# Kernel optimization log

Measured on AMD Instinct MI355X. Metric: run time of the kernel, lower is better.

The kernel has to match this reference:

```python
import jax, jax.numpy as jnp
import numpy as np

N_NODES = 10000

def _gcn_norm(edges, n_nodes):
    # PyG GCNConv default: add self-loops, symmetric normalization D^-1/2 A_hat D^-1/2
    src, dst = edges[0], edges[1]
    loop = jnp.arange(n_nodes, dtype=src.dtype)
    src = jnp.concatenate([src, loop])
    dst = jnp.concatenate([dst, loop])
    deg = jax.ops.segment_sum(jnp.ones_like(dst, dtype=jnp.float32), dst, num_segments=n_nodes)
    dinv = jnp.where(deg > 0, jax.lax.rsqrt(deg), 0.0)
    norm = dinv[src] * dinv[dst]  # [E + N]
    return src, dst, norm

def _gcn_layer(x, src, dst, norm, W, b):
    # linear transform, then gather -> weight -> scatter-add aggregation
    x = x @ W  # [N, F]
    msg = x[src] * norm[:, None]  # [E+N, F]
    out = jax.ops.segment_sum(msg, dst, num_segments=x.shape[0])
    return out + b

def setup_inputs() -> dict:
    key = jax.random.key(0)
    k1, k2, k3, k4 = jax.random.split(key, 4)
    d = 128
    E = 640000
    scale = 1.0 / np.sqrt(d)
    return {
        "nodes_embeddings": jax.random.normal(k1, (N_NODES, d), dtype=jnp.float32),
        "edges": jax.random.randint(k2, (2, E), 0, N_NODES, dtype=jnp.int64),
        "W1": jax.random.normal(k3, (d, d), dtype=jnp.float32) * scale,
        "b1": jnp.zeros((d,), dtype=jnp.float32),
        "W2": jax.random.normal(k4, (d, d), dtype=jnp.float32) * scale,
        "b2": jnp.zeros((d,), dtype=jnp.float32),
    }

def reference(nodes_embeddings, edges, W1, b1, W2, b2):
    src, dst, norm = _gcn_norm(edges, nodes_embeddings.shape[0])
    x = _gcn_layer(nodes_embeddings, src, dst, norm, W1, b1)
    x = _gcn_layer(x, src, dst, norm, W2, b2)
    return x
```

## Files before the change

### kernel.cpp

```cpp
#include <hip/hip_runtime.h>
#include <hip/hip_bf16.h>

#define D 128
#define NBINS 157
#define BIN_CAP 5120
#define EPB 4096
#define SCAP 96
#define SLABW (NBINS * SCAP)

__device__ __forceinline__ unsigned rne_bf16(float f) {
    unsigned u = __float_as_uint(f);
    return (u + 0x7FFFu + ((u >> 16) & 1u)) >> 16;
}
__device__ __forceinline__ float bf16_lo(unsigned u) { return __uint_as_float(u << 16); }
__device__ __forceinline__ float bf16_hi(unsigned u) { return __uint_as_float(u & 0xFFFF0000u); }

__global__ __launch_bounds__(512) void fused_gemm_scatter(
        const float* __restrict__ X, const float* __restrict__ W,
        float* __restrict__ Y,
        const int* __restrict__ src, const int* __restrict__ dst,
        int* __restrict__ cntMat, int* __restrict__ binned,
        int E, int N, int gGemm) {
    __shared__ float smem[D * D];
    int tid = threadIdx.x;

    if ((int)blockIdx.x < gGemm) {
        {
            const float4* W4 = (const float4*)W;
            float4* Ws4 = (float4*)smem;
            #pragma unroll
            for (int i = 0; i < 8; ++i)
                Ws4[tid + 512 * i] = W4[tid + 512 * i];
        }
        __syncthreads();
        const float2* Ws2 = (const float2*)smem;
        int col2 = tid & 63;
        int wv   = __builtin_amdgcn_readfirstlane(tid >> 6);
        int row0 = blockIdx.x * 32 + wv * 4;
        if (row0 >= N) return;

        const float4* xr[4];
        #pragma unroll
        for (int r = 0; r < 4; ++r) {
            int rr = row0 + r; if (rr > N - 1) rr = N - 1;
            xr[r] = (const float4*)(X + (size_t)rr * D);
        }
        float accx[4] = {0.f, 0.f, 0.f, 0.f};
        float accy[4] = {0.f, 0.f, 0.f, 0.f};
        #pragma unroll 8
        for (int kb = 0; kb < 32; ++kb) {
            float4 xv[4];
            #pragma unroll
            for (int r = 0; r < 4; ++r) xv[r] = xr[r][kb];
            #pragma unroll
            for (int kk = 0; kk < 4; ++kk) {
                float2 w = Ws2[(4 * kb + kk) * 64 + col2];
                #pragma unroll
                for (int r = 0; r < 4; ++r) {
                    float xs = ((const float*)&xv[r])[kk];
                    accx[r] = fmaf(xs, w.x, accx[r]);
                    accy[r] = fmaf(xs, w.y, accy[r]);
                }
            }
        }
        #pragma unroll
        for (int r = 0; r < 4; ++r) {
            int rr = row0 + r;
            if (rr < N)
                ((float2*)Y)[(size_t)rr * 64 + col2] = make_float2(accx[r], accy[r]);
        }
    } else {
        int* cnt   = (int*)smem;
        int* loff  = cnt + 160;
        int* scur  = cnt + 320;
        int* stage = cnt + 480;
        for (int b = tid; b < NBINS; b += 512) cnt[b] = 0;
        __syncthreads();

        int bid = blockIdx.x - gGemm;
        int base = bid * EPB + tid * 8;
        int s[8], dl[8], bn[8];
        int ne = 0;
        if (base + 8 <= E) {
            const int4* s4 = (const int4*)(src + base);
            const int4* d4 = (const int4*)(dst + base);
            int4 a0 = s4[0], a1 = s4[1], c0 = d4[0], c1 = d4[1];
            int ss[8] = {a0.x, a0.y, a0.z, a0.w, a1.x, a1.y, a1.z, a1.w};
            int dd[8] = {c0.x, c0.y, c0.z, c0.w, c1.x, c1.y, c1.z, c1.w};
            ne = 8;
            #pragma unroll
            for (int i = 0; i < 8; ++i) { s[i] = ss[i]; bn[i] = dd[i] >> 6; dl[i] = dd[i] & 63; }
        } else {
            for (int i = 0; i < 8; ++i) {
                int e = base + i;
                if (e < E) { s[ne] = src[e]; int d = dst[e]; bn[ne] = d >> 6; dl[ne] = d & 63; ++ne; }
            }
        }
        for (int i = 0; i < ne; ++i) atomicAdd(&cnt[bn[i]], 1);
        __syncthreads();

        if (tid < 64) {
            int c0 = (3 * tid     < NBINS) ? cnt[3 * tid    ] : 0;
            int c1 = (3 * tid + 1 < NBINS) ? cnt[3 * tid + 1] : 0;
            int c2 = (3 * tid + 2 < NBINS) ? cnt[3 * tid + 2] : 0;
            int tsum = c0 + c1 + c2;
            int incl = tsum;
            #pragma unroll
            for (int off = 1; off < 64; off <<= 1) {
                int t = __shfl_up(incl, off);
                if (tid >= off) incl += t;
            }
            int excl = incl - tsum;
            if (3 * tid < NBINS)     { loff[3 * tid]     = excl;           scur[3 * tid]     = excl; }
            if (3 * tid + 1 < NBINS) { loff[3 * tid + 1] = excl + c0;      scur[3 * tid + 1] = excl + c0; }
            if (3 * tid + 2 < NBINS) { loff[3 * tid + 2] = excl + c0 + c1; scur[3 * tid + 2] = excl + c0 + c1; }
        }
        __syncthreads();

        for (int i = 0; i < ne; ++i) {
            int p = atomicAdd(&scur[bn[i]], 1);
            stage[p] = s[i] | (dl[i] << 14);
        }
        __syncthreads();

        int wv = tid >> 6, lane = tid & 63;
        for (int b = wv; b < NBINS; b += 8) {
            int n = cnt[b], so = loff[b];
            int* dstp = binned + b * SLABW + bid * SCAP;
            for (int i = lane; i < n; i += 64) dstp[i] = stage[so + i];
            if (lane == 0) cntMat[b * NBINS + bid] = n;
        }
    }
}

__global__ __launch_bounds__(1024) void sort_bins(const int* __restrict__ cntMat,
                                                  const int* __restrict__ binned,
                                                  unsigned short* __restrict__ csr16,
                                                  float* __restrict__ dinv,
                                                  int* __restrict__ nodeStart,
                                                  int* __restrict__ nodeEnd,
                                                  const float* __restrict__ Y,
                                                  unsigned* __restrict__ Zb,
                                                  unsigned* __restrict__ Zb2, int N) {
    __shared__ int h[16][64];
    __shared__ int cur[16][64];
    __shared__ int scnt[NBINS];
    __shared__ float sdinv[64];
    __shared__ int padTot;
    __shared__ int stage[BIN_CAP];
    int b = blockIdx.x, tid = threadIdx.x;
    int wv = tid >> 6, lane = tid & 63;
    h[wv][lane] = 0;
    if (tid < NBINS) scnt[tid] = cntMat[b * NBINS + tid];
    __syncthreads();
    const int* binBase = binned + b * SLABW;
    for (int s = wv; s < NBINS; s += 16) {
        int n = scnt[s];
        const int* sp = binBase + s * SCAP;
        for (int i = lane; i < n; i += 64) atomicAdd(&h[wv][sp[i] >> 14], 1);
    }
    __syncthreads();
    if (tid < 64) {
        int hv[16];
        int deg = 0;
        #pragma unroll
        for (int w2 = 0; w2 < 16; ++w2) { hv[w2] = h[w2][tid]; deg += hv[w2]; }
        int pdeg = (deg + 7) & ~7;
        int incl = pdeg;
        #pragma unroll
        for (int off = 1; off < 64; off <<= 1) {
            int t = __shfl_up(incl, off);
            if (tid >= off) incl += t;
        }
        int excl = incl - pdeg;
        int run = excl;
        #pragma unroll
        for (int w2 = 0; w2 < 16; ++w2) { cur[w2][tid] = run; run += hv[w2]; }
        float dv = rsqrtf((float)(deg + 1));
        sdinv[tid] = dv;
        if (tid == 63) padTot = incl;
        int node = b * 64 + tid;
        if (node < N) {
            dinv[node]      = dv;
            nodeStart[node] = b * BIN_CAP + excl;
            nodeEnd[node]   = b * BIN_CAP + excl + pdeg;
        }
    }
    __syncthreads();
    int cntPad = padTot;
    for (int i = tid; i < cntPad; i += 1024) stage[i] = N;
    __syncthreads();
    for (int s = wv; s < NBINS; s += 16) {
        int n = scnt[s];
        const int* sp = binBase + s * SCAP;
        for (int i = lane; i < n; i += 64) {
            int p = sp[i];
            int pos = atomicAdd(&cur[wv][p >> 14], 1);
            stage[pos] = p & 0x3FFF;
        }
    }
    {
        const float4* Y4 = (const float4*)Y;
        uint2* Zp = (uint2*)Zb;
        #pragma unroll
        for (int i = 0; i < 2; ++i) {
            int idx = tid + 1024 * i;
            int row = idx >> 5, c = idx & 31;
            int node = b * 64 + row;
            if (node < N) {
                float4 v = Y4[(size_t)node * 32 + c];
                float dv = sdinv[row];
                uint2 o;
                o.x = (rne_bf16(v.y * dv) << 16) | rne_bf16(v.x * dv);
                o.y = (rne_bf16(v.w * dv) << 16) | rne_bf16(v.z * dv);
                Zp[(size_t)node * 32 + c] = o;
            }
        }
    }
    if (b == 0 && tid < 64) {
        Zb [(size_t)N * 64 + tid] = 0u;
        Zb2[(size_t)N * 64 + tid] = 0u;
    }
    __syncthreads();
    unsigned short* bw = csr16 + b * BIN_CAP;
    for (int i = tid; i < cntPad; i += 1024) bw[i] = (unsigned short)stage[i];
}

__global__ __launch_bounds__(256) void aggregate(const unsigned* __restrict__ Zb,
                                                 const int* __restrict__ nodeStart,
                                                 const int* __restrict__ nodeEnd,
                                                 const unsigned short* __restrict__ csr16,
                                                 const float* __restrict__ dinv,
                                                 const float* __restrict__ bias,
                                                 float* __restrict__ Out, int N,
                                                 const float* __restrict__ W2,
                                                 unsigned* __restrict__ Zout) {
    __shared__ float rowsLds[4][128];
    const bool fused = (W2 != nullptr);
    int wv   = __builtin_amdgcn_readfirstlane(threadIdx.x >> 6);
    int node = blockIdx.x * 4 + wv;
    bool active = (node < N);
    if (!fused && !active) return;
    int lane = threadIdx.x & 63;
    int l16  = lane & 15;
    const uint4* Z4 = (const uint4*)Zb;

    if (active) {
        int g = lane >> 4;
        float f0=0.f,f1=0.f,f2=0.f,f3=0.f,f4=0.f,f5=0.f,f6=0.f,f7=0.f;

        int e = nodeStart[node], end = nodeEnd[node];
        while (e < end) {
            int rem = end - e; int cnt = rem > 64 ? 64 : rem;
            int my = (lane < cnt) ? (int)csr16[e + lane] : N;
            int rounds = cnt >> 2;
            #pragma unroll 16
            for (int j = 0; j < rounds; ++j) {
                int idx = __shfl(my, j * 4 + g);
                uint4 u = Z4[idx * 16 + l16];
                f0 += bf16_lo(u.x); f1 += bf16_hi(u.x);
                f2 += bf16_lo(u.y); f3 += bf16_hi(u.y);
                f4 += bf16_lo(u.z); f5 += bf16_hi(u.z);
                f6 += bf16_lo(u.w); f7 += bf16_hi(u.w);
            }
            e += cnt;
        }
        #pragma unroll
        for (int m = 16; m <= 32; m <<= 1) {
            f0 += __shfl_xor(f0, m); f1 += __shfl_xor(f1, m);
            f2 += __shfl_xor(f2, m); f3 += __shfl_xor(f3, m);
            f4 += __shfl_xor(f4, m); f5 += __shfl_xor(f5, m);
            f6 += __shfl_xor(f6, m); f7 += __shfl_xor(f7, m);
        }
        if (lane < 16) {
            uint4 su = Z4[node * 16 + l16];
            float dv = dinv[node];
            const float4* bp4 = (const float4*)bias;
            float4 ba = bp4[l16 * 2], bb = bp4[l16 * 2 + 1];
            float4 o0, o1;
            o0.x = (f0 + bf16_lo(su.x)) * dv + ba.x;
            o0.y = (f1 + bf16_hi(su.x)) * dv + ba.y;
            o0.z = (f2 + bf16_lo(su.y)) * dv + ba.z;
            o0.w = (f3 + bf16_hi(su.y)) * dv + ba.w;
            o1.x = (f4 + bf16_lo(su.z)) * dv + bb.x;
            o1.y = (f5 + bf16_hi(su.z)) * dv + bb.y;
            o1.z = (f6 + bf16_lo(su.w)) * dv + bb.z;
            o1.w = (f7 + bf16_hi(su.w)) * dv + bb.w;
            if (fused) {
                float4* rp = (float4*)&rowsLds[wv][0];
                rp[l16 * 2]     = o0;
                rp[l16 * 2 + 1] = o1;
            } else {
                float4* op = (float4*)Out + (size_t)node * 32 + l16 * 2;
                op[0] = o0;
                op[1] = o1;
            }
        }
    }

    if (fused) {
        __syncthreads();
        int tid  = threadIdx.x;
        int r    = tid >> 6;
        int col2 = (tid & 63) << 1;
        int node2 = blockIdx.x * 4 + r;
        const float* xrow = &rowsLds[r][0];
        float ac0 = 0.f, ac1 = 0.f;
        #pragma unroll 8
        for (int k = 0; k < 128; ++k) {
            float xs = xrow[k];
            float2 w2v = *(const float2*)(W2 + (size_t)k * D + col2);
            ac0 = fmaf(xs, w2v.x, ac0);
            ac1 = fmaf(xs, w2v.y, ac1);
        }
        if (node2 < N) {
            float dv = dinv[node2];
            Zout[(size_t)node2 * 64 + (tid & 63)] =
                (rne_bf16(ac1 * dv) << 16) | rne_bf16(ac0 * dv);
        }
    }
}

extern "C" void kernel_launch(void* const* d_in, const int* in_sizes, int n_in,
                              void* d_out, int out_size, void* d_ws, size_t ws_size,
                              hipStream_t stream) {
    const float* X  = (const float*)d_in[0];
    const int*   ed = (const int*)d_in[1];
    const float* W1 = (const float*)d_in[2];
    const float* b1 = (const float*)d_in[3];
    const float* W2 = (const float*)d_in[4];
    const float* b2 = (const float*)d_in[5];
    float* out = (float*)d_out;

    const int N = in_sizes[0] / D;
    const int E = in_sizes[1] / 2;
    const int* src = ed;
    const int* dst = ed + E;

    char* w = (char*)d_ws;
    float*    Y        = (float*)w;            w += (size_t)N * D * sizeof(float);
    unsigned* Zb       = (unsigned*)w;         w += (size_t)(N + 1) * 64 * sizeof(unsigned);
    unsigned* Zb2      = (unsigned*)w;         w += (size_t)(N + 1) * 64 * sizeof(unsigned);
    int*      binned   = (int*)w;              w += (size_t)NBINS * SLABW * sizeof(int);
    unsigned short* csr16 = (unsigned short*)w; w += (size_t)NBINS * BIN_CAP * sizeof(unsigned short);
    float*    dinv     = (float*)w;            w += (size_t)N * sizeof(float);
    int*      nodeStart= (int*)w;              w += (size_t)N * sizeof(int);
    int*      nodeEnd  = (int*)w;              w += (size_t)N * sizeof(int);
    int*      cntMat   = (int*)w;              w += (size_t)NBINS * NBINS * sizeof(int);

    int gGemm1 = (N + 31) / 32;
    int gScat  = (E + EPB - 1) / EPB;
    fused_gemm_scatter<<<gGemm1 + gScat, 512, 0, stream>>>(
        X, W1, Y, src, dst, cntMat, binned, E, N, gGemm1);
    sort_bins<<<NBINS, 1024, 0, stream>>>(cntMat, binned, csr16, dinv,
                                          nodeStart, nodeEnd, Y, Zb, Zb2, N);

    int gAgg = (N + 3) / 4;
    aggregate<<<gAgg, 256, 0, stream>>>(Zb, nodeStart, nodeEnd, csr16, dinv,
                                        b1, out, N, W2, Zb2);
    aggregate<<<gAgg, 256, 0, stream>>>(Zb2, nodeStart, nodeEnd, csr16, dinv,
                                        b2, out, N, nullptr, nullptr);
}
```

Baseline: 152.2 us.

## Aggregate four nodes per wave and widen the fused W2 GEMM tile

Each wavefront now gathers neighbour rows for four nodes at once, interleaving four independent load streams to raise memory-level parallelism, and each block covers 16 nodes instead of 4. The fused second-layer GEMM now computes 8 output columns per thread over 16 rows, so each W2 load is reused across more FMAs. In exchange, register pressure rises sharply from 32 accumulators, and a wave's loop runs for as long as its highest-degree node, wasting lanes when degrees differ.

```diff
diff --git a/kernel.cpp b/kernel.cpp
--- a/kernel.cpp
+++ b/kernel.cpp
@@ -235,11 +235,11 @@
                                                  float* __restrict__ Out, int N,
                                                  const float* __restrict__ W2,
                                                  unsigned* __restrict__ Zout) {
-    __shared__ float rowsLds[4][128];
+    __shared__ float rowsLds[16][128];
     const bool fused = (W2 != nullptr);
-    int wv   = __builtin_amdgcn_readfirstlane(threadIdx.x >> 6);
-    int node = blockIdx.x * 4 + wv;
-    bool active = (node < N);
+    int wv    = __builtin_amdgcn_readfirstlane(threadIdx.x >> 6);
+    int node0 = blockIdx.x * 16 + wv * 4;
+    bool active = (node0 < N);
     if (!fused && !active) return;
     int lane = threadIdx.x & 63;
     int l16  = lane & 15;
@@ -247,47 +247,104 @@
 
     if (active) {
         int g = lane >> 4;
-        float f0=0.f,f1=0.f,f2=0.f,f3=0.f,f4=0.f,f5=0.f,f6=0.f,f7=0.f;
-
-        int e = nodeStart[node], end = nodeEnd[node];
-        while (e < end) {
-            int rem = end - e; int cnt = rem > 64 ? 64 : rem;
-            int my = (lane < cnt) ? (int)csr16[e + lane] : N;
-            int rounds = cnt >> 2;
+        float a0=0.f,a1=0.f,a2=0.f,a3=0.f,a4=0.f,a5=0.f,a6=0.f,a7=0.f;
+        float b0=0.f,b1=0.f,b2=0.f,b3=0.f,b4=0.f,b5=0.f,b6=0.f,b7=0.f;
+        float c0=0.f,c1=0.f,c2=0.f,c3=0.f,c4=0.f,c5=0.f,c6=0.f,c7=0.f;
+        float d0=0.f,d1=0.f,d2=0.f,d3=0.f,d4=0.f,d5=0.f,d6=0.f,d7=0.f;
+
+        int e0 = nodeStart[node0], end0 = nodeEnd[node0];
+        int e1 = 0, end1 = 0, e2 = 0, end2 = 0, e3 = 0, end3 = 0;
+        if (node0 + 1 < N) { e1 = nodeStart[node0 + 1]; end1 = nodeEnd[node0 + 1]; }
+        if (node0 + 2 < N) { e2 = nodeStart[node0 + 2]; end2 = nodeEnd[node0 + 2]; }
+        if (node0 + 3 < N) { e3 = nodeStart[node0 + 3]; end3 = nodeEnd[node0 + 3]; }
+
+        while (e0 < end0 || e1 < end1 || e2 < end2 || e3 < end3) {
+            int r0 = end0 - e0; int cnt0 = r0 > 64 ? 64 : (r0 > 0 ? r0 : 0);
+            int r1 = end1 - e1; int cnt1 = r1 > 64 ? 64 : (r1 > 0 ? r1 : 0);
+            int r2 = end2 - e2; int cnt2 = r2 > 64 ? 64 : (r2 > 0 ? r2 : 0);
+            int r3 = end3 - e3; int cnt3 = r3 > 64 ? 64 : (r3 > 0 ? r3 : 0);
+            int my0 = (lane < cnt0) ? (int)csr16[e0 + lane] : N;
+            int my1 = (lane < cnt1) ? (int)csr16[e1 + lane] : N;
+            int my2 = (lane < cnt2) ? (int)csr16[e2 + lane] : N;
+            int my3 = (lane < cnt3) ? (int)csr16[e3 + lane] : N;
+            int cm01 = cnt0 > cnt1 ? cnt0 : cnt1;
+            int cm23 = cnt2 > cnt3 ? cnt2 : cnt3;
+            int cmax = cm01 > cm23 ? cm01 : cm23;
+            int rounds = cmax >> 2;
             #pragma unroll 16
             for (int j = 0; j < rounds; ++j) {
-                int idx = __shfl(my, j * 4 + g);
-                uint4 u = Z4[idx * 16 + l16];
-                f0 += bf16_lo(u.x); f1 += bf16_hi(u.x);
-                f2 += bf16_lo(u.y); f3 += bf16_hi(u.y);
-                f4 += bf16_lo(u.z); f5 += bf16_hi(u.z);
-                f6 += bf16_lo(u.w); f7 += bf16_hi(u.w);
-            }
-            e += cnt;
+                int i0 = __shfl(my0, j * 4 + g);
+                int i1 = __shfl(my1, j * 4 + g);
+                int i2 = __shfl(my2, j * 4 + g);
+                int i3 = __shfl(my3, j * 4 + g);
+                uint4 u0 = Z4[i0 * 16 + l16];
+                uint4 u1 = Z4[i1 * 16 + l16];
+                uint4 u2 = Z4[i2 * 16 + l16];
+                uint4 u3 = Z4[i3 * 16 + l16];
+                a0 += bf16_lo(u0.x); a1 += bf16_hi(u0.x);
+                a2 += bf16_lo(u0.y); a3 += bf16_hi(u0.y);
+                a4 += bf16_lo(u0.z); a5 += bf16_hi(u0.z);
+                a6 += bf16_lo(u0.w); a7 += bf16_hi(u0.w);
+                b0 += bf16_lo(u1.x); b1 += bf16_hi(u1.x);
+                b2 += bf16_lo(u1.y); b3 += bf16_hi(u1.y);
+                b4 += bf16_lo(u1.z); b5 += bf16_hi(u1.z);
+                b6 += bf16_lo(u1.w); b7 += bf16_hi(u1.w);
+                c0 += bf16_lo(u2.x); c1 += bf16_hi(u2.x);
+                c2 += bf16_lo(u2.y); c3 += bf16_hi(u2.y);
+                c4 += bf16_lo(u2.z); c5 += bf16_hi(u2.z);
+                c6 += bf16_lo(u2.w); c7 += bf16_hi(u2.w);
+                d0 += bf16_lo(u3.x); d1 += bf16_hi(u3.x);
+                d2 += bf16_lo(u3.y); d3 += bf16_hi(u3.y);
+                d4 += bf16_lo(u3.z); d5 += bf16_hi(u3.z);
+                d6 += bf16_lo(u3.w); d7 += bf16_hi(u3.w);
+            }
+            e0 += cnt0; e1 += cnt1; e2 += cnt2; e3 += cnt3;
         }
         #pragma unroll
         for (int m = 16; m <= 32; m <<= 1) {
-            f0 += __shfl_xor(f0, m); f1 += __shfl_xor(f1, m);
-            f2 += __shfl_xor(f2, m); f3 += __shfl_xor(f3, m);
-            f4 += __shfl_xor(f4, m); f5 += __shfl_xor(f5, m);
-            f6 += __shfl_xor(f6, m); f7 += __shfl_xor(f7, m);
-        }
-        if (lane < 16) {
+            a0 += __shfl_xor(a0, m); a1 += __shfl_xor(a1, m);
+            a2 += __shfl_xor(a2, m); a3 += __shfl_xor(a3, m);
+            a4 += __shfl_xor(a4, m); a5 += __shfl_xor(a5, m);
+            a6 += __shfl_xor(a6, m); a7 += __shfl_xor(a7, m);
+            b0 += __shfl_xor(b0, m); b1 += __shfl_xor(b1, m);
+            b2 += __shfl_xor(b2, m); b3 += __shfl_xor(b3, m);
+            b4 += __shfl_xor(b4, m); b5 += __shfl_xor(b5, m);
+            b6 += __shfl_xor(b6, m); b7 += __shfl_xor(b7, m);
+            c0 += __shfl_xor(c0, m); c1 += __shfl_xor(c1, m);
+            c2 += __shfl_xor(c2, m); c3 += __shfl_xor(c3, m);
+            c4 += __shfl_xor(c4, m); c5 += __shfl_xor(c5, m);
+            c6 += __shfl_xor(c6, m); c7 += __shfl_xor(c7, m);
+            d0 += __shfl_xor(d0, m); d1 += __shfl_xor(d1, m);
+            d2 += __shfl_xor(d2, m); d3 += __shfl_xor(d3, m);
+            d4 += __shfl_xor(d4, m); d5 += __shfl_xor(d5, m);
+            d6 += __shfl_xor(d6, m); d7 += __shfl_xor(d7, m);
+        }
+        int half = lane >> 4;
+        int node = node0 + half;
+        if (node < N) {
+            float s0 = half==0 ? a0 : half==1 ? b0 : half==2 ? c0 : d0;
+            float s1 = half==0 ? a1 : half==1 ? b1 : half==2 ? c1 : d1;
+            float s2 = half==0 ? a2 : half==1 ? b2 : half==2 ? c2 : d2;
+            float s3 = half==0 ? a3 : half==1 ? b3 : half==2 ? c3 : d3;
+            float s4 = half==0 ? a4 : half==1 ? b4 : half==2 ? c4 : d4;
+            float s5 = half==0 ? a5 : half==1 ? b5 : half==2 ? c5 : d5;
+            float s6 = half==0 ? a6 : half==1 ? b6 : half==2 ? c6 : d6;
+            float s7 = half==0 ? a7 : half==1 ? b7 : half==2 ? c7 : d7;
             uint4 su = Z4[node * 16 + l16];
             float dv = dinv[node];
             const float4* bp4 = (const float4*)bias;
             float4 ba = bp4[l16 * 2], bb = bp4[l16 * 2 + 1];
             float4 o0, o1;
-            o0.x = (f0 + bf16_lo(su.x)) * dv + ba.x;
-            o0.y = (f1 + bf16_hi(su.x)) * dv + ba.y;
-            o0.z = (f2 + bf16_lo(su.y)) * dv + ba.z;
-            o0.w = (f3 + bf16_hi(su.y)) * dv + ba.w;
-            o1.x = (f4 + bf16_lo(su.z)) * dv + bb.x;
-            o1.y = (f5 + bf16_hi(su.z)) * dv + bb.y;
-            o1.z = (f6 + bf16_lo(su.w)) * dv + bb.z;
-            o1.w = (f7 + bf16_hi(su.w)) * dv + bb.w;
+            o0.x = (s0 + bf16_lo(su.x)) * dv + ba.x;
+            o0.y = (s1 + bf16_hi(su.x)) * dv + ba.y;
+            o0.z = (s2 + bf16_lo(su.y)) * dv + ba.z;
+            o0.w = (s3 + bf16_hi(su.y)) * dv + ba.w;
+            o1.x = (s4 + bf16_lo(su.z)) * dv + bb.x;
+            o1.y = (s5 + bf16_hi(su.z)) * dv + bb.y;
+            o1.z = (s6 + bf16_lo(su.w)) * dv + bb.z;
+            o1.w = (s7 + bf16_hi(su.w)) * dv + bb.w;
             if (fused) {
-                float4* rp = (float4*)&rowsLds[wv][0];
+                float4* rp = (float4*)&rowsLds[wv * 4 + half][0];
                 rp[l16 * 2]     = o0;
                 rp[l16 * 2 + 1] = o1;
             } else {
@@ -301,22 +358,33 @@
     if (fused) {
         __syncthreads();
         int tid  = threadIdx.x;
-        int r    = tid >> 6;
-        int col2 = (tid & 63) << 1;
-        int node2 = blockIdx.x * 4 + r;
+        int r    = tid >> 4;
+        int c8   = (tid & 15) << 3;
+        int node2 = blockIdx.x * 16 + r;
         const float* xrow = &rowsLds[r][0];
-        float ac0 = 0.f, ac1 = 0.f;
+        float ac0=0.f,ac1=0.f,ac2=0.f,ac3=0.f,ac4=0.f,ac5=0.f,ac6=0.f,ac7=0.f;
         #pragma unroll 8
         for (int k = 0; k < 128; ++k) {
             float xs = xrow[k];
-            float2 w2v = *(const float2*)(W2 + (size_t)k * D + col2);
-            ac0 = fmaf(xs, w2v.x, ac0);
-            ac1 = fmaf(xs, w2v.y, ac1);
+            float4 wa = *(const float4*)(W2 + (size_t)k * D + c8);
+            float4 wb = *(const float4*)(W2 + (size_t)k * D + c8 + 4);
+            ac0 = fmaf(xs, wa.x, ac0);
+            ac1 = fmaf(xs, wa.y, ac1);
+            ac2 = fmaf(xs, wa.z, ac2);
+            ac3 = fmaf(xs, wa.w, ac3);
+            ac4 = fmaf(xs, wb.x, ac4);
+            ac5 = fmaf(xs, wb.y, ac5);
+            ac6 = fmaf(xs, wb.z, ac6);
+            ac7 = fmaf(xs, wb.w, ac7);
         }
         if (node2 < N) {
             float dv = dinv[node2];
-            Zout[(size_t)node2 * 64 + (tid & 63)] =
-                (rne_bf16(ac1 * dv) << 16) | rne_bf16(ac0 * dv);
+            uint4 o;
+            o.x = (rne_bf16(ac1 * dv) << 16) | rne_bf16(ac0 * dv);
+            o.y = (rne_bf16(ac3 * dv) << 16) | rne_bf16(ac2 * dv);
+            o.z = (rne_bf16(ac5 * dv) << 16) | rne_bf16(ac4 * dv);
+            o.w = (rne_bf16(ac7 * dv) << 16) | rne_bf16(ac6 * dv);
+            ((uint4*)Zout)[(size_t)node2 * 16 + (tid & 15)] = o;
         }
     }
 }
@@ -355,7 +423,7 @@
     sort_bins<<<NBINS, 1024, 0, stream>>>(cntMat, binned, csr16, dinv,
                                           nodeStart, nodeEnd, Y, Zb, Zb2, N);
 
-    int gAgg = (N + 3) / 4;
+    int gAgg = (N + 15) / 16;
     aggregate<<<gAgg, 256, 0, stream>>>(Zb, nodeStart, nodeEnd, csr16, dinv,
                                         b1, out, N, W2, Zb2);
     aggregate<<<gAgg, 256, 0, stream>>>(Zb2, nodeStart, nodeEnd, csr16, dinv,
```

New measurement: 141.8 us. 6.8% less time.
